# Kernel tuning notes

Measured on AMD Instinct MI355X. Metric: run time of the kernel, lower is better.

The kernel has to match this reference:

```python
import jax, jax.numpy as jnp
import numpy as np

B, C, H, W = 8, 512, 32, 32
NUM_HEADS = 8


def setup_inputs() -> dict:
    key = jax.random.key(0)
    ks = jax.random.split(key, 7)
    s = 0.02
    return {
        "x": jax.random.normal(ks[0], (B, C, H, W), dtype=jnp.float32),
        "Wq": jax.random.normal(ks[1], (C, C), dtype=jnp.float32) * s,
        "bq": jax.random.normal(ks[2], (C,), dtype=jnp.float32) * s,
        "Wk": jax.random.normal(ks[3], (C, C), dtype=jnp.float32) * s,
        "bk": jax.random.normal(ks[4], (C,), dtype=jnp.float32) * s,
        "Wv": jax.random.normal(ks[5], (C, C), dtype=jnp.float32) * s,
        "bv": jax.random.normal(ks[6], (C,), dtype=jnp.float32) * s,
        "gamma": jnp.zeros((1,), dtype=jnp.float32),
    }


def reference(x, Wq, bq, Wk, bk, Wv, bv, gamma):
    b, c, h, w = x.shape
    nh = NUM_HEADS
    hd = c // nh
    n = h * w

    def proj(Wt, bt):
        # 1x1 conv == per-pixel linear: [b,c,h,w] x [o,c] -> [b,o,h,w]
        return jnp.einsum('bchw,oc->bohw', x, Wt) + bt[None, :, None, None]

    q = proj(Wq, bq).reshape(b, nh, hd, n).transpose(0, 1, 3, 2)  # [b,nh,n,hd]
    k = proj(Wk, bk).reshape(b, nh, hd, n)                         # [b,nh,hd,n]
    v = proj(Wv, bv).reshape(b, nh, hd, n).transpose(0, 1, 3, 2)   # [b,nh,n,hd]

    energy = jnp.einsum('bhnd,bhdm->bhnm', q, k)  # NOTE: no 1/sqrt(d) scale (faithful)
    attention = jax.nn.softmax(energy, axis=-1)
    out = jnp.einsum('bhnm,bhmd->bhnd', attention, v)  # [b,nh,n,hd]
    out = out.transpose(0, 1, 3, 2).reshape(b, c, h, w)
    return gamma * out + x
```

## Files before the change

### kernel.cpp

```cpp
#include <hip/hip_runtime.h>
#include <cstdint>
#include <cstddef>

typedef float floatx4 __attribute__((ext_vector_type(4)));
typedef short shortx4 __attribute__((ext_vector_type(4)));
typedef short shortx8 __attribute__((ext_vector_type(8)));

#define LDS_AS __attribute__((address_space(3)))
#define GLB_AS __attribute__((address_space(1)))

#define MFMA_16x16x32_BF16(A, B, C) __builtin_amdgcn_mfma_f32_16x16x32_bf16(A, B, C, 0, 0, 0)

#if defined(__HIP_DEVICE_COMPILE__)
  #if __has_builtin(__builtin_amdgcn_mfma_f32_16x16x16bf16_1k)
    #define MFMA_16x16x16_BF16(A, B, C) __builtin_amdgcn_mfma_f32_16x16x16bf16_1k(A, B, C, 0, 0, 0)
  #else
    #error "gfx950 device pass lacks __builtin_amdgcn_mfma_f32_16x16x16bf16_1k"
  #endif
#else
  #define MFMA_16x16x16_BF16(A, B, C) (C)
#endif

__device__ __forceinline__ unsigned short f2bf(float f) {
    unsigned int u = __float_as_uint(f);
    u += 0x7fffu + ((u >> 16) & 1u);
    return (unsigned short)(u >> 16);
}

__device__ __forceinline__ void gll16(const void* g, void* l) {
    __builtin_amdgcn_global_load_lds((const GLB_AS uint32_t*)g, (LDS_AS uint32_t*)l, 16, 0, 0);
}


__global__ __launch_bounds__(256) void prep_kernel(
    const float* __restrict__ x,
    const float* __restrict__ Wq, const float* __restrict__ Wk, const float* __restrict__ Wv,
    unsigned short* __restrict__ xT, unsigned short* __restrict__ Wb)
{
    const int bid = blockIdx.x;
    const int t = threadIdx.x;
    if (bid < 1024) {
        __shared__ alignas(16) unsigned short sT[64][72];
        const int b = bid >> 7, rem = bid & 127;
        const int c0 = (rem >> 4) * 64, p0 = (rem & 15) * 64;
        const int cl = (t >> 4) * 4, p4 = (t & 15) * 4;
        float4 v[4];
#pragma unroll
        for (int di = 0; di < 4; ++di)
            v[di] = *(const float4*)(x + (size_t)(b * 512 + c0 + cl + di) * 1024 + p0 + p4);
#pragma unroll
        for (int j = 0; j < 4; ++j) {
            shortx4 pk;
#pragma unroll
            for (int dd = 0; dd < 4; ++dd)
                pk[dd] = (short)f2bf(((const float*)&v[dd])[j]);
            *(shortx4*)&sT[p4 + j][cl] = pk;
        }
        __syncthreads();
        const int p = t >> 2, ch = (t & 3) * 16;
        const size_t base = ((size_t)b * 1024 + p0 + p) * 512 + c0 + ch;
        *(shortx8*)&xT[base] = *(const shortx8*)&sT[p][ch];
        *(shortx8*)&xT[base + 8] = *(const shortx8*)&sT[p][ch + 8];
    } else {
        const int wb = bid - 1024;
        const int mat = wb >> 6;
        const float* src = (mat == 0) ? Wq : (mat == 1) ? Wk : Wv;
        const int off0 = (wb & 63) * 4096;
#pragma unroll
        for (int r = 0; r < 4; ++r) {
            const int idx = off0 + r * 1024 + t * 4;
            const float4 v = *(const float4*)(src + idx);
            shortx4 pk;
            pk[0] = (short)f2bf(v.x); pk[1] = (short)f2bf(v.y);
            pk[2] = (short)f2bf(v.z); pk[3] = (short)f2bf(v.w);
            *(shortx4*)&Wb[(size_t)mat * 262144 + idx] = pk;
        }
    }
}

__global__ __launch_bounds__(256, 2) void proj_kernel(
    const unsigned short* __restrict__ Wb, const unsigned short* __restrict__ xT,
    const float* __restrict__ bq, const float* __restrict__ bk, const float* __restrict__ bv,
    unsigned short* __restrict__ Qg, unsigned short* __restrict__ Kg,
    unsigned short* __restrict__ Vg)
{
    __shared__ union {
        struct { unsigned short W[2][3][64][64]; unsigned short X[2][128][64]; } s;
        unsigned short Ep[128][72];
    } u;

    const int tid = threadIdx.x;
    const int w = tid >> 6, lane = tid & 63;
    const int quad = lane >> 4, l16 = lane & 15;
    const int wo = w & 1, wp = w >> 1;
    const int bh = blockIdx.x, b = bh >> 3, h = bh & 7;
    const int p0 = blockIdx.y * 128;
    const int o0 = h * 64;

    floatx4 acc[3][2][4];
#pragma unroll
    for (int t = 0; t < 3; ++t) {
        const float* bsrc = (t == 0) ? bq : (t == 1) ? bk : bv;
#pragma unroll
        for (int ot = 0; ot < 2; ++ot) {
            floatx4 bi;
#pragma unroll
            for (int i = 0; i < 4; ++i)
                bi[i] = bsrc[o0 + wo * 32 + ot * 16 + quad * 4 + i];
#pragma unroll
            for (int pt = 0; pt < 4; ++pt) acc[t][ot][pt] = bi;
        }
    }

    auto stage = [&](int ks, int bfi) {
        const int c0 = ks * 64;
#pragma unroll
        for (int ii = 0; ii < 6; ++ii) {
            const int rf0 = w * 48 + ii * 8;
            const int rf = rf0 + (lane >> 3);
            const int mt = rf >> 6, r = rf & 63;
            const int cl = (lane & 7) ^ (r & 7);
            gll16(Wb + (size_t)mt * 262144 + (size_t)(o0 + r) * 512 + c0 + cl * 8,
                  &u.s.W[bfi][0][0][0] + rf0 * 64);
        }
#pragma unroll
        for (int ii = 0; ii < 4; ++ii) {
            const int r0 = w * 32 + ii * 8;
            const int r = r0 + (lane >> 3);
            const int cl = (lane & 7) ^ (r & 7);
            gll16(xT + (size_t)(b * 1024 + p0 + r) * 512 + c0 + cl * 8,
                  &u.s.X[bfi][0][0] + r0 * 64);
        }
    };

    stage(0, 0);
    for (int ks = 0; ks < 8; ++ks) {
        __syncthreads();
        if (ks + 1 < 8) stage(ks + 1, (ks + 1) & 1);
        const int bfi = ks & 1;
#pragma unroll
        for (int kc = 0; kc < 2; ++kc) {
            shortx8 af[3][2], bx[4];
#pragma unroll
            for (int t = 0; t < 3; ++t)
#pragma unroll
                for (int ot = 0; ot < 2; ++ot) {
                    const int r = wo * 32 + ot * 16 + l16;
                    const int pc = (kc * 4 + quad) ^ (r & 7);
                    af[t][ot] = *(const shortx8*)&u.s.W[bfi][t][r][pc * 8];
                }
#pragma unroll
            for (int pt = 0; pt < 4; ++pt) {
                const int r = wp * 64 + pt * 16 + l16;
                const int pc = (kc * 4 + quad) ^ (r & 7);
                bx[pt] = *(const shortx8*)&u.s.X[bfi][r][pc * 8];
            }
#pragma unroll
            for (int t = 0; t < 3; ++t)
#pragma unroll
                for (int ot = 0; ot < 2; ++ot)
#pragma unroll
                    for (int pt = 0; pt < 4; ++pt)
                        acc[t][ot][pt] = MFMA_16x16x32_BF16(af[t][ot], bx[pt], acc[t][ot][pt]);
        }
    }

#pragma unroll
    for (int ot = 0; ot < 2; ++ot)
#pragma unroll
        for (int pt = 0; pt < 4; ++pt)
#pragma unroll
            for (int i = 0; i < 4; ++i) {
                const int d = wo * 32 + ot * 16 + quad * 4 + i;
                const int p = p0 + wp * 64 + pt * 16 + l16;
                Vg[((size_t)bh * 64 + d) * 1024 + p] = f2bf(acc[2][ot][pt][i]);
            }
#pragma unroll
    for (int t = 0; t < 2; ++t) {
        __syncthreads();
#pragma unroll
        for (int ot = 0; ot < 2; ++ot)
#pragma unroll
            for (int pt = 0; pt < 4; ++pt)
#pragma unroll
                for (int i = 0; i < 4; ++i)
                    u.Ep[wp * 64 + pt * 16 + l16][wo * 32 + ot * 16 + quad * 4 + i] =
                        f2bf(acc[t][ot][pt][i]);
        __syncthreads();
        unsigned short* G = (t == 0) ? Qg : Kg;
        const int p = tid >> 1, ch = (tid & 1) * 32;
        const size_t base = ((size_t)bh * 1024 + p0 + p) * 64 + ch;
#pragma unroll
        for (int jj = 0; jj < 4; ++jj)
            *(shortx8*)&G[base + jj * 8] = *(const shortx8*)&u.Ep[p][ch + jj * 8];
    }
}

__global__ __launch_bounds__(256, 2) void attn_kernel(
    const unsigned short* __restrict__ Qg, const unsigned short* __restrict__ Kg,
    const unsigned short* __restrict__ Vg, const float* __restrict__ x,
    const float* __restrict__ gamma, float* __restrict__ out)
{
    __shared__ alignas(16) unsigned short sK[2][64][64];
    __shared__ alignas(16) unsigned short sV[2][64][64];

    const int tid = threadIdx.x;
    const int w = tid >> 6, lane = tid & 63;
    const int quad = lane >> 4, l16 = lane & 15;
    const int bh = blockIdx.x, b = bh >> 3, h = bh & 7;
    const int p0 = blockIdx.y * 128;
    const int pw = p0 + w * 32;

    shortx8 aq[2][2];
#pragma unroll
    for (int pt = 0; pt < 2; ++pt)
#pragma unroll
        for (int ks = 0; ks < 2; ++ks)
            aq[pt][ks] = *(const shortx8*)
                &Qg[((size_t)bh * 1024 + pw + pt * 16 + l16) * 64 + ks * 32 + quad * 8];

    floatx4 oacc[2][4];
#pragma unroll
    for (int pt = 0; pt < 2; ++pt)
#pragma unroll
        for (int dt = 0; dt < 4; ++dt) oacc[pt][dt] = (floatx4)0.0f;
    float m_run[2] = {-__builtin_huge_valf(), -__builtin_huge_valf()};
    float l_run[2] = {0.0f, 0.0f};

    auto stage = [&](int kt, int bfi) {
        const int m0 = kt * 64;
#pragma unroll
        for (int kv = 0; kv < 2; ++kv) {
            const int r0 = w * 16 + kv * 8;
            const int r = r0 + (lane >> 3);
            const int cl = (lane & 7) ^ (r & 7);
            gll16(Kg + ((size_t)bh * 1024 + m0 + r) * 64 + cl * 8, &sK[bfi][0][0] + r0 * 64);
            gll16(Vg + ((size_t)bh * 64 + r) * 1024 + m0 + cl * 8, &sV[bfi][0][0] + r0 * 64);
        }
    };

    stage(0, 0);
    for (int kt = 0; kt < 16; ++kt) {
        __syncthreads();
        if (kt + 1 < 16) stage(kt + 1, (kt + 1) & 1);
        const int bfi = kt & 1;

        floatx4 s[2][4];
#pragma unroll
        for (int pt = 0; pt < 2; ++pt)
#pragma unroll
            for (int nt = 0; nt < 4; ++nt) s[pt][nt] = (floatx4)0.0f;
#pragma unroll
        for (int nt = 0; nt < 4; ++nt)
#pragma unroll
            for (int ks = 0; ks < 2; ++ks) {
                const int r = nt * 16 + l16;
                const int pc = (ks * 4 + quad) ^ (r & 7);
                const shortx8 ak = *(const shortx8*)&sK[bfi][r][pc * 8];
#pragma unroll
                for (int pt = 0; pt < 2; ++pt)
                    s[pt][nt] = MFMA_16x16x32_BF16(ak, aq[pt][ks], s[pt][nt]);
            }

        float al[2];
#pragma unroll
        for (int pt = 0; pt < 2; ++pt) {
            float rm = -__builtin_huge_valf();
#pragma unroll
            for (int nt = 0; nt < 4; ++nt)
#pragma unroll
                for (int i = 0; i < 4; ++i) rm = fmaxf(rm, s[pt][nt][i]);
            rm = fmaxf(rm, __shfl_xor(rm, 16));
            rm = fmaxf(rm, __shfl_xor(rm, 32));
            const float mnew = fmaxf(m_run[pt], rm);
            al[pt] = __expf(m_run[pt] - mnew);
            m_run[pt] = mnew;
            float rs = 0.0f;
#pragma unroll
            for (int nt = 0; nt < 4; ++nt)
#pragma unroll
                for (int i = 0; i < 4; ++i) {
                    const float pv = __expf(s[pt][nt][i] - mnew);
                    s[pt][nt][i] = pv;
                    rs += pv;
                }
            rs += __shfl_xor(rs, 16);
            rs += __shfl_xor(rs, 32);
            l_run[pt] = l_run[pt] * al[pt] + rs;
#pragma unroll
            for (int dt = 0; dt < 4; ++dt) oacc[pt][dt] *= al[pt];
        }

        shortx4 bp[2][4];
#pragma unroll
        for (int pt = 0; pt < 2; ++pt)
#pragma unroll
            for (int mt = 0; mt < 4; ++mt) {
                shortx4 pk;
#pragma unroll
                for (int j = 0; j < 4; ++j) pk[j] = (short)f2bf(s[pt][mt][j]);
                bp[pt][mt] = pk;
            }

#pragma unroll
        for (int dt = 0; dt < 4; ++dt)
#pragma unroll
            for (int mt = 0; mt < 4; ++mt) {
                const int r = dt * 16 + l16;
                const int pc = (mt * 2 + (quad >> 1)) ^ (r & 7);
                const shortx4 av = *(const shortx4*)&sV[bfi][r][pc * 8 + (quad & 1) * 4];
#pragma unroll
                for (int pt = 0; pt < 2; ++pt)
                    oacc[pt][dt] = MFMA_16x16x16_BF16(av, bp[pt][mt], oacc[pt][dt]);
            }
    }

    const float g = gamma[0];
    const float invl[2] = {1.0f / l_run[0], 1.0f / l_run[1]};
#pragma unroll
    for (int pt = 0; pt < 2; ++pt)
#pragma unroll
        for (int dt = 0; dt < 4; ++dt)
#pragma unroll
            for (int i = 0; i < 4; ++i) {
                const int d = dt * 16 + quad * 4 + i;
                const int p = pw + pt * 16 + l16;
                const size_t idx = ((size_t)b * 512 + h * 64 + d) * 1024 + p;
                out[idx] = g * (oacc[pt][dt][i] * invl[pt]) + x[idx];
            }
}

extern "C" void kernel_launch(void* const* d_in, const int* in_sizes, int n_in,
                              void* d_out, int out_size, void* d_ws, size_t ws_size,
                              hipStream_t stream) {
    const float* x     = (const float*)d_in[0];
    const float* Wq    = (const float*)d_in[1];
    const float* bq    = (const float*)d_in[2];
    const float* Wk    = (const float*)d_in[3];
    const float* bk    = (const float*)d_in[4];
    const float* Wv    = (const float*)d_in[5];
    const float* bv    = (const float*)d_in[6];
    const float* gamma = (const float*)d_in[7];
    float* out = (float*)d_out;

    unsigned short* xT = (unsigned short*)d_ws;
    unsigned short* Wb = xT + 4194304;
    unsigned short* Qg = Wb + 786432;
    unsigned short* Kg = Qg + 4194304;
    unsigned short* Vg = Kg + 4194304;

    prep_kernel<<<1216, 256, 0, stream>>>(x, Wq, Wk, Wv, xT, Wb);
    proj_kernel<<<dim3(64, 8), 256, 0, stream>>>(Wb, xT, bq, bk, bv, Qg, Kg, Vg);
    attn_kernel<<<dim3(64, 8), 256, 0, stream>>>(Qg, Kg, Vg, x, gamma, out);
}
```

Measured before the change: 146.3 us.

## Split projection over output halves, fold log2e into Q, use exp2 and MFMA row sums

The projection kernel is re-tiled to a 32-wide output slice and a 32-wide K step, launched over a third grid dimension. This doubles the block count and cuts per-block registers and LDS, and launch bounds are raised to allow four blocks per CU. Q is pre-scaled by log2(e) so attention can use the hardware exp2 builtin, and the softmax probabilities are packed with the native cvt_pk_bf16 instruction. Row sums now come from an extra MFMA against a ones vector instead of shuffles. In exchange, the rounding of the probabilities changes (the fallback path truncates instead of rounding), the denominators are computed from bf16-rounded values, and the projection does twice as many K-loop iterations, each with smaller tiles.

```diff
diff --git a/kernel.cpp b/kernel.cpp
--- a/kernel.cpp
+++ b/kernel.cpp
@@ -3,8 +3,10 @@
 #include <cstddef>
 
 typedef float floatx4 __attribute__((ext_vector_type(4)));
+typedef short shortx2 __attribute__((ext_vector_type(2)));
 typedef short shortx4 __attribute__((ext_vector_type(4)));
 typedef short shortx8 __attribute__((ext_vector_type(8)));
+typedef int   intx2  __attribute__((ext_vector_type(2)));
 
 #define LDS_AS __attribute__((address_space(3)))
 #define GLB_AS __attribute__((address_space(1)))
@@ -21,10 +23,37 @@
   #define MFMA_16x16x16_BF16(A, B, C) (C)
 #endif
 
+#define LOG2E 1.44269504088896340736f
+
 __device__ __forceinline__ unsigned short f2bf(float f) {
     unsigned int u = __float_as_uint(f);
     u += 0x7fffu + ((u >> 16) & 1u);
     return (unsigned short)(u >> 16);
+}
+
+__device__ __forceinline__ float exp2f_fast(float x) {
+#if defined(__HIP_DEVICE_COMPILE__) && __has_builtin(__builtin_amdgcn_exp2f)
+    return __builtin_amdgcn_exp2f(x);
+#else
+    return exp2f(x);
+#endif
+}
+
+__device__ __forceinline__ shortx4 pk4(float a, float b, float c, float d) {
+#if defined(__HIP_DEVICE_COMPILE__) && __has_builtin(__builtin_amdgcn_cvt_pk_bf16_f32)
+    typedef __bf16 bf16x2_t __attribute__((ext_vector_type(2)));
+    bf16x2_t lo = __builtin_amdgcn_cvt_pk_bf16_f32(a, b);
+    bf16x2_t hi = __builtin_amdgcn_cvt_pk_bf16_f32(c, d);
+    intx2 p; p[0] = __builtin_bit_cast(int, lo); p[1] = __builtin_bit_cast(int, hi);
+    return __builtin_bit_cast(shortx4, p);
+#else
+    unsigned int ua = __float_as_uint(a), ub = __float_as_uint(b);
+    unsigned int uc = __float_as_uint(c), ud = __float_as_uint(d);
+    intx2 p;
+    p[0] = (int)((ua >> 16) | (ub & 0xffff0000u));
+    p[1] = (int)((uc >> 16) | (ud & 0xffff0000u));
+    return __builtin_bit_cast(shortx4, p);
+#endif
 }
 
 __device__ __forceinline__ void gll16(const void* g, void* l) {
@@ -78,26 +107,26 @@
     }
 }
 
-__global__ __launch_bounds__(256, 2) void proj_kernel(
+__global__ __launch_bounds__(256, 4) void proj_kernel(
     const unsigned short* __restrict__ Wb, const unsigned short* __restrict__ xT,
     const float* __restrict__ bq, const float* __restrict__ bk, const float* __restrict__ bv,
     unsigned short* __restrict__ Qg, unsigned short* __restrict__ Kg,
     unsigned short* __restrict__ Vg)
 {
     __shared__ union {
-        struct { unsigned short W[2][3][64][64]; unsigned short X[2][128][64]; } s;
-        unsigned short Ep[128][72];
+        struct { unsigned short W[2][3][32][32]; unsigned short X[2][128][32]; } s;
+        unsigned short Ep[128][40];
     } u;
 
     const int tid = threadIdx.x;
     const int w = tid >> 6, lane = tid & 63;
     const int quad = lane >> 4, l16 = lane & 15;
-    const int wo = w & 1, wp = w >> 1;
     const int bh = blockIdx.x, b = bh >> 3, h = bh & 7;
     const int p0 = blockIdx.y * 128;
-    const int o0 = h * 64;
-
-    floatx4 acc[3][2][4];
+    const int oo = blockIdx.z;
+    const int o0 = h * 64 + oo * 32;
+
+    floatx4 acc[3][2][2];
 #pragma unroll
     for (int t = 0; t < 3; ++t) {
         const float* bsrc = (t == 0) ? bq : (t == 1) ? bk : bv;
@@ -106,93 +135,91 @@
             floatx4 bi;
 #pragma unroll
             for (int i = 0; i < 4; ++i)
-                bi[i] = bsrc[o0 + wo * 32 + ot * 16 + quad * 4 + i];
-#pragma unroll
-            for (int pt = 0; pt < 4; ++pt) acc[t][ot][pt] = bi;
+                bi[i] = bsrc[o0 + ot * 16 + quad * 4 + i];
+#pragma unroll
+            for (int pt = 0; pt < 2; ++pt) acc[t][ot][pt] = bi;
         }
     }
 
     auto stage = [&](int ks, int bfi) {
-        const int c0 = ks * 64;
-#pragma unroll
-        for (int ii = 0; ii < 6; ++ii) {
-            const int rf0 = w * 48 + ii * 8;
-            const int rf = rf0 + (lane >> 3);
-            const int mt = rf >> 6, r = rf & 63;
-            const int cl = (lane & 7) ^ (r & 7);
-            gll16(Wb + (size_t)mt * 262144 + (size_t)(o0 + r) * 512 + c0 + cl * 8,
-                  &u.s.W[bfi][0][0][0] + rf0 * 64);
-        }
-#pragma unroll
-        for (int ii = 0; ii < 4; ++ii) {
-            const int r0 = w * 32 + ii * 8;
-            const int r = r0 + (lane >> 3);
-            const int cl = (lane & 7) ^ (r & 7);
-            gll16(xT + (size_t)(b * 1024 + p0 + r) * 512 + c0 + cl * 8,
-                  &u.s.X[bfi][0][0] + r0 * 64);
+        const int c0 = ks * 32;
+#pragma unroll
+        for (int jj = 0; jj < 4; ++jj) {
+            const int j = jj * 4 + w;
+            if (j < 6) {
+                const int rf0 = j * 16;
+                const int rf = rf0 + (lane >> 2);
+                const int mt = rf >> 5, r = rf & 31;
+                const int cl = (lane & 3) ^ (r & 3);
+                gll16(Wb + (size_t)mt * 262144 + (size_t)(o0 + r) * 512 + c0 + cl * 8,
+                      &u.s.W[bfi][0][0][0] + rf0 * 32);
+            } else if (j < 14) {
+                const int r0 = (j - 6) * 16;
+                const int r = r0 + (lane >> 2);
+                const int cl = (lane & 3) ^ (r & 3);
+                gll16(xT + (size_t)(b * 1024 + p0 + r) * 512 + c0 + cl * 8,
+                      &u.s.X[bfi][0][0] + r0 * 32);
+            }
         }
     };
 
     stage(0, 0);
-    for (int ks = 0; ks < 8; ++ks) {
-        __syncthreads();
-        if (ks + 1 < 8) stage(ks + 1, (ks + 1) & 1);
+    for (int ks = 0; ks < 16; ++ks) {
+        __syncthreads();
+        if (ks + 1 < 16) stage(ks + 1, (ks + 1) & 1);
         const int bfi = ks & 1;
-#pragma unroll
-        for (int kc = 0; kc < 2; ++kc) {
-            shortx8 af[3][2], bx[4];
-#pragma unroll
-            for (int t = 0; t < 3; ++t)
-#pragma unroll
-                for (int ot = 0; ot < 2; ++ot) {
-                    const int r = wo * 32 + ot * 16 + l16;
-                    const int pc = (kc * 4 + quad) ^ (r & 7);
-                    af[t][ot] = *(const shortx8*)&u.s.W[bfi][t][r][pc * 8];
-                }
-#pragma unroll
-            for (int pt = 0; pt < 4; ++pt) {
-                const int r = wp * 64 + pt * 16 + l16;
-                const int pc = (kc * 4 + quad) ^ (r & 7);
-                bx[pt] = *(const shortx8*)&u.s.X[bfi][r][pc * 8];
-            }
-#pragma unroll
-            for (int t = 0; t < 3; ++t)
-#pragma unroll
-                for (int ot = 0; ot < 2; ++ot)
-#pragma unroll
-                    for (int pt = 0; pt < 4; ++pt)
-                        acc[t][ot][pt] = MFMA_16x16x32_BF16(af[t][ot], bx[pt], acc[t][ot][pt]);
-        }
+        shortx8 af[3][2], bx[2];
+#pragma unroll
+        for (int t = 0; t < 3; ++t)
+#pragma unroll
+            for (int ot = 0; ot < 2; ++ot) {
+                const int r = ot * 16 + l16;
+                const int pc = quad ^ (r & 3);
+                af[t][ot] = *(const shortx8*)&u.s.W[bfi][t][r][pc * 8];
+            }
+#pragma unroll
+        for (int pt = 0; pt < 2; ++pt) {
+            const int r = w * 32 + pt * 16 + l16;
+            const int pc = quad ^ (r & 3);
+            bx[pt] = *(const shortx8*)&u.s.X[bfi][r][pc * 8];
+        }
+#pragma unroll
+        for (int t = 0; t < 3; ++t)
+#pragma unroll
+            for (int ot = 0; ot < 2; ++ot)
+#pragma unroll
+                for (int pt = 0; pt < 2; ++pt)
+                    acc[t][ot][pt] = MFMA_16x16x32_BF16(af[t][ot], bx[pt], acc[t][ot][pt]);
     }
 
 #pragma unroll
     for (int ot = 0; ot < 2; ++ot)
 #pragma unroll
-        for (int pt = 0; pt < 4; ++pt)
+        for (int pt = 0; pt < 2; ++pt)
 #pragma unroll
             for (int i = 0; i < 4; ++i) {
-                const int d = wo * 32 + ot * 16 + quad * 4 + i;
-                const int p = p0 + wp * 64 + pt * 16 + l16;
+                const int d = oo * 32 + ot * 16 + quad * 4 + i;
+                const int p = p0 + w * 32 + pt * 16 + l16;
                 Vg[((size_t)bh * 64 + d) * 1024 + p] = f2bf(acc[2][ot][pt][i]);
             }
 #pragma unroll
     for (int t = 0; t < 2; ++t) {
+        const float scale = (t == 0) ? LOG2E : 1.0f;
         __syncthreads();
 #pragma unroll
         for (int ot = 0; ot < 2; ++ot)
 #pragma unroll
-            for (int pt = 0; pt < 4; ++pt)
+            for (int pt = 0; pt < 2; ++pt)
 #pragma unroll
                 for (int i = 0; i < 4; ++i)
-                    u.Ep[wp * 64 + pt * 16 + l16][wo * 32 + ot * 16 + quad * 4 + i] =
-                        f2bf(acc[t][ot][pt][i]);
+                    u.Ep[w * 32 + pt * 16 + l16][ot * 16 + quad * 4 + i] =
+                        f2bf(acc[t][ot][pt][i] * scale);
         __syncthreads();
         unsigned short* G = (t == 0) ? Qg : Kg;
-        const int p = tid >> 1, ch = (tid & 1) * 32;
-        const size_t base = ((size_t)bh * 1024 + p0 + p) * 64 + ch;
-#pragma unroll
-        for (int jj = 0; jj < 4; ++jj)
-            *(shortx8*)&G[base + jj * 8] = *(const shortx8*)&u.Ep[p][ch + jj * 8];
+        const int p = tid >> 1, ch = (tid & 1) * 16;
+        const size_t base = ((size_t)bh * 1024 + p0 + p) * 64 + oo * 32 + ch;
+        *(shortx8*)&G[base]     = *(const shortx8*)&u.Ep[p][ch];
+        *(shortx8*)&G[base + 8] = *(const shortx8*)&u.Ep[p][ch + 8];
     }
 }
 
@@ -226,6 +253,7 @@
         for (int dt = 0; dt < 4; ++dt) oacc[pt][dt] = (floatx4)0.0f;
     float m_run[2] = {-__builtin_huge_valf(), -__builtin_huge_valf()};
     float l_run[2] = {0.0f, 0.0f};
+    const shortx4 ones4 = {(short)0x3F80, (short)0x3F80, (short)0x3F80, (short)0x3F80};
 
     auto stage = [&](int kt, int bfi) {
         const int m0 = kt * 64;
@@ -273,20 +301,13 @@
             rm = fmaxf(rm, __shfl_xor(rm, 16));
             rm = fmaxf(rm, __shfl_xor(rm, 32));
             const float mnew = fmaxf(m_run[pt], rm);
-            al[pt] = __expf(m_run[pt] - mnew);
+            al[pt] = exp2f_fast(m_run[pt] - mnew);
             m_run[pt] = mnew;
-            float rs = 0.0f;
 #pragma unroll
             for (int nt = 0; nt < 4; ++nt)
 #pragma unroll
-                for (int i = 0; i < 4; ++i) {
-                    const float pv = __expf(s[pt][nt][i] - mnew);
-                    s[pt][nt][i] = pv;
-                    rs += pv;
-                }
-            rs += __shfl_xor(rs, 16);
-            rs += __shfl_xor(rs, 32);
-            l_run[pt] = l_run[pt] * al[pt] + rs;
+                for (int i = 0; i < 4; ++i)
+                    s[pt][nt][i] = exp2f_fast(s[pt][nt][i] - mnew);
 #pragma unroll
             for (int dt = 0; dt < 4; ++dt) oacc[pt][dt] *= al[pt];
         }
@@ -295,13 +316,10 @@
 #pragma unroll
         for (int pt = 0; pt < 2; ++pt)
 #pragma unroll
-            for (int mt = 0; mt < 4; ++mt) {
-                shortx4 pk;
-#pragma unroll
-                for (int j = 0; j < 4; ++j) pk[j] = (short)f2bf(s[pt][mt][j]);
-                bp[pt][mt] = pk;
-            }
-
+            for (int mt = 0; mt < 4; ++mt)
+                bp[pt][mt] = pk4(s[pt][mt][0], s[pt][mt][1], s[pt][mt][2], s[pt][mt][3]);
+
+        floatx4 lac[2] = {(floatx4)0.0f, (floatx4)0.0f};
 #pragma unroll
         for (int dt = 0; dt < 4; ++dt)
 #pragma unroll
@@ -313,6 +331,14 @@
                 for (int pt = 0; pt < 2; ++pt)
                     oacc[pt][dt] = MFMA_16x16x16_BF16(av, bp[pt][mt], oacc[pt][dt]);
             }
+#pragma unroll
+        for (int mt = 0; mt < 4; ++mt)
+#pragma unroll
+            for (int pt = 0; pt < 2; ++pt)
+                lac[pt] = MFMA_16x16x16_BF16(ones4, bp[pt][mt], lac[pt]);
+#pragma unroll
+        for (int pt = 0; pt < 2; ++pt)
+            l_run[pt] = l_run[pt] * al[pt] + lac[pt][0];
     }
 
     const float g = gamma[0];
@@ -350,6 +376,6 @@
     unsigned short* Vg = Kg + 4194304;
 
     prep_kernel<<<1216, 256, 0, stream>>>(x, Wq, Wk, Wv, xT, Wb);
-    proj_kernel<<<dim3(64, 8), 256, 0, stream>>>(Wb, xT, bq, bk, bv, Qg, Kg, Vg);
+    proj_kernel<<<dim3(64, 8, 2), 256, 0, stream>>>(Wb, xT, bq, bk, bv, Qg, Kg, Vg);
     attn_kernel<<<dim3(64, 8), 256, 0, stream>>>(Qg, Kg, Vg, x, gamma, out);
 }
```

Measured after the change: 135.4 us. 7.5% less time.
